# Performance work log

Measured on AMD Instinct MI355X. Metric: run time of the kernel, lower is better.

Reference implementation:

```python
import jax, jax.numpy as jnp
import numpy as np
from jax import lax

B, C, IMG, PATCH = 128, 3, 224, 16
EMB, HEADS = 384, 6
NPATCH = (IMG // PATCH) ** 2          # 196
NTOK = NPATCH + 1                     # 197 (cls token)
HID = int(EMB * 4.0)                  # 1536 (also expert hidden)
NE, K = 4, 2                          # num_experts (hardcoded 4), top-k
NCLS = 1000


def _ln(x, g, b, eps=1e-5):
    m = jnp.mean(x, axis=-1, keepdims=True)
    v = jnp.mean((x - m) ** 2, axis=-1, keepdims=True)
    return (x - m) * lax.rsqrt(v + eps) * g + b


def setup_inputs() -> dict:
    key = jax.random.key(0)
    ks = jax.random.split(key, 16)
    s = 0.02
    return {
        "x": jax.random.normal(ks[0], (B, C, IMG, IMG), jnp.float32),
        "conv_w": jax.random.normal(ks[1], (EMB, C, PATCH, PATCH), jnp.float32) * s,
        "conv_b": jnp.zeros((EMB,), jnp.float32),
        "cls_token": jax.random.normal(ks[2], (1, 1, EMB), jnp.float32) * s,
        "pos_embed": jax.random.normal(ks[3], (1, NTOK, EMB), jnp.float32) * s,
        "ln1_g": jnp.ones((EMB,), jnp.float32),
        "ln1_b": jnp.zeros((EMB,), jnp.float32),
        "in_proj_w": jax.random.normal(ks[4], (3 * EMB, EMB), jnp.float32) * s,
        "in_proj_b": jnp.zeros((3 * EMB,), jnp.float32),
        "out_proj_w": jax.random.normal(ks[5], (EMB, EMB), jnp.float32) * s,
        "out_proj_b": jnp.zeros((EMB,), jnp.float32),
        "router_w": jax.random.normal(ks[6], (NE, EMB), jnp.float32) * s,
        "router_b": jnp.zeros((NE,), jnp.float32),
        "ew1": jax.random.normal(ks[7], (NE, EMB, HID), jnp.float32) * s,
        "eb1": jnp.zeros((NE, HID), jnp.float32),
        "ew2": jax.random.normal(ks[8], (NE, HID, EMB), jnp.float32) * s,
        "eb2": jnp.zeros((NE, EMB), jnp.float32),
        "ln2_g": jnp.ones((EMB,), jnp.float32),
        "ln2_b": jnp.zeros((EMB,), jnp.float32),
        "head_w": jax.random.normal(ks[9], (NCLS, EMB), jnp.float32) * s,
        "head_b": jnp.zeros((NCLS,), jnp.float32),
    }


def reference(x, conv_w, conv_b, cls_token, pos_embed,
              ln1_g, ln1_b, in_proj_w, in_proj_b, out_proj_w, out_proj_b,
              router_w, router_b, ew1, eb1, ew2, eb2,
              ln2_g, ln2_b, head_w, head_b):
    # ---- patch embedding: Conv2d(stride=kernel=patch) -> [B, N, E]
    h = lax.conv_general_dilated(x, conv_w, window_strides=(PATCH, PATCH),
                                 padding="VALID",
                                 dimension_numbers=("NCHW", "OIHW", "NCHW"))
    h = h + conv_b[None, :, None, None]
    h = h.reshape(B, EMB, NPATCH).transpose(0, 2, 1)          # [B, 196, E]
    h = jnp.concatenate([jnp.broadcast_to(cls_token, (B, 1, EMB)), h], axis=1)
    h = h + pos_embed                                         # [B, 197, E]

    # ---- SelfAttentionBlock (NOTE: no residual; same LN applied twice, as in source)
    hn = _ln(h, ln1_g, ln1_b)
    qkv = hn @ in_proj_w.T + in_proj_b                        # [B, N, 3E]
    q, k, v = jnp.split(qkv, 3, axis=-1)
    hd = EMB // HEADS
    q = q.reshape(B, NTOK, HEADS, hd)
    k = k.reshape(B, NTOK, HEADS, hd)
    v = v.reshape(B, NTOK, HEADS, hd)
    att = jnp.einsum("bqhd,bkhd->bhqk", q, k) / np.sqrt(hd).astype(np.float32)
    att = jax.nn.softmax(att, axis=-1)
    o = jnp.einsum("bhqk,bkhd->bqhd", att, v).reshape(B, NTOK, EMB)
    o = o @ out_proj_w.T + out_proj_b
    h = _ln(o, ln1_g, ln1_b)                                  # second LN, same params

    # ---- MoE: dense all-expert FFN + top-k gather + mean
    scores = jax.nn.softmax(h @ router_w.T + router_b, axis=-1)   # [B, N, NE]
    topk_vals, topk_idx = lax.top_k(scores, K)                    # [B, N, K]
    flat = h.reshape(B * NTOK, EMB)
    eh = jax.nn.gelu(jnp.einsum("te,neh->tnh", flat, ew1) + eb1, approximate=False)
    eo = jnp.einsum("tnh,nhe->tne", eh, ew2) + eb2                # [BN, NE, E]
    idx = topk_idx.reshape(B * NTOK, K, 1)
    sel = jnp.take_along_axis(eo, idx, axis=1)                    # [BN, K, E]
    h = sel.mean(axis=1).reshape(B, NTOK, EMB)

    # ---- final norm + classification head on cls token
    h = _ln(h, ln2_g, ln2_b)
    return h[:, 0] @ head_w.T + head_b                            # [B, NCLS]
```

## Files before the change

kernel.cpp:

```cpp
#include <hip/hip_runtime.h>
#include <cstdint>
#include <cstddef>

typedef _Float16 f16;
typedef _Float16 f16x2 __attribute__((ext_vector_type(2)));
typedef _Float16 f16x8 __attribute__((ext_vector_type(8)));
typedef float    f32x4 __attribute__((ext_vector_type(4)));

constexpr int NTOKC  = 197;
constexpr int TTOK   = 128 * 197;
constexpr int EMB    = 384;
constexpr int HID    = 1536;

constexpr size_t OFF_CONVW   = 0;
constexpr size_t OFF_EW1T    = 1179648;
constexpr size_t OFF_EW2T    = 5898240;
constexpr size_t OFF_HEADW16 = 10616832;
constexpr size_t OFF_XCLS16  = 11403264;
constexpr size_t OFF_HCLS16  = 11799552;
constexpr size_t OFF_MASKW   = 11897856;
constexpr size_t OFF_EH      = 11899904;
constexpr size_t OFF_EPART   = 13472768;
constexpr size_t OFF_HFIN    = 16618496;
constexpr size_t OFF_XH      = 16716800;
constexpr size_t OFF_R       = 36082688;
constexpr size_t OFF_CVEC    = 36094976;
constexpr size_t OFF_U16     = 36099072;
constexpr size_t OFF_SG      = 38212608;
constexpr size_t OFF_SCLS    = 38817792;
constexpr size_t OFF_F       = 38818816;
constexpr size_t OFF_B2      = 40588288;
constexpr size_t OFF_FPART   = 40589824;
constexpr size_t WS_NEEDED   = 41769472;

__device__ __forceinline__ void gload16(const void* g, void* l) {
  __builtin_amdgcn_global_load_lds(
      (__attribute__((address_space(1))) void*)(void*)g,
      (__attribute__((address_space(3))) void*)l, 16, 0, 0);
}

#define PACK8(hv, p0, p1) { hv[0]=(f16)p0.x; hv[1]=(f16)p0.y; hv[2]=(f16)p0.z; hv[3]=(f16)p0.w; \
                            hv[4]=(f16)p1.x; hv[5]=(f16)p1.y; hv[6]=(f16)p1.z; hv[7]=(f16)p1.w; }

__global__ __launch_bounds__(256) void prep_all_k(
    const float* __restrict__ conv_w, const float* __restrict__ head_w,
    const float* __restrict__ ew1, const float* __restrict__ ew2,
    const float* __restrict__ inp_w, const float* __restrict__ inp_b,
    const float* __restrict__ outp_w, const float* __restrict__ outp_b,
    f16* __restrict__ convw, f16* __restrict__ headw16,
    f16* __restrict__ ew1t, f16* __restrict__ ew2t,
    f16* __restrict__ F, float* __restrict__ bias2) {
  __shared__ __attribute__((aligned(16))) char sbuf[4352];
  const int bx = (int)blockIdx.x, tid = threadIdx.x;
  if (bx < 2688) {
    int i = bx * 256 + tid;
    if (i < 294912) convw[i] = (f16)conv_w[i];
    int j = i - 294912;
    if (j >= 0 && j < 393216) {
      int row = j / 384;
      headw16[j] = (row < 1000) ? (f16)head_w[j] : (f16)0.f;
    }
  } else if (bx < 4992) {
    float (*tile)[33] = (float(*)[33])sbuf;
    int local = bx - 2688;
    int e = local / 576, r2 = local - e * 576;
    int byy = r2 / 48, bxx = r2 - byy * 48;
    const float* pin = ew1 + (size_t)e * 384 * 1536;
    f16* pout = ew1t + (size_t)e * 384 * 1536;
    int c0 = bxx * 32, r0 = byy * 32;
    int tx = tid & 31, ty = tid >> 5;
#pragma unroll
    for (int i = 0; i < 4; i++)
      tile[ty + 8 * i][tx] = pin[(size_t)(r0 + ty + 8 * i) * 1536 + c0 + tx];
    __syncthreads();
#pragma unroll
    for (int i = 0; i < 4; i++)
      pout[(size_t)(c0 + ty + 8 * i) * 384 + r0 + tx] = (f16)tile[tx][ty + 8 * i];
  } else if (bx < 7296) {
    float (*tile)[33] = (float(*)[33])sbuf;
    int local = bx - 4992;
    int e = local / 576, r2 = local - e * 576;
    int byy = r2 / 12, bxx = r2 - byy * 12;
    const float* pin = ew2 + (size_t)e * 1536 * 384;
    f16* pout = ew2t + (size_t)e * 1536 * 384;
    int c0 = bxx * 32, r0 = byy * 32;
    int tx = tid & 31, ty = tid >> 5;
#pragma unroll
    for (int i = 0; i < 4; i++)
      tile[ty + 8 * i][tx] = pin[(size_t)(r0 + ty + 8 * i) * 384 + c0 + tx];
    __syncthreads();
#pragma unroll
    for (int i = 0; i < 4; i++)
      pout[(size_t)(c0 + ty + 8 * i) * 1536 + r0 + tx] = (f16)tile[tx][ty + 8 * i];
  } else if (bx < 7440) {
    float (*wo)[64] = (float(*)[64])sbuf;
    int local = bx - 7296;
    int h = local / 24, nt = local - h * 24;
    int n0 = nt * 16;
    for (int i = tid; i < 1024; i += 256) {
      int ni = i >> 6, d = i & 63;
      wo[ni][d] = outp_w[(size_t)(n0 + ni) * 384 + h * 64 + d];
    }
    __syncthreads();
    for (int e = tid; e < 6144; e += 256) {
      int ni = e / 384, k2 = e - ni * 384;
      const float* wv = inp_w + (size_t)(768 + h * 64) * 384 + k2;
      float a = 0.f;
#pragma unroll 8
      for (int d = 0; d < 64; d++) a += wo[ni][d] * wv[(size_t)d * 384];
      F[(size_t)(n0 + ni) * 2304 + h * 384 + k2] = (f16)a;
    }
  } else {
    int nt = bx - 7440;
    if (tid < 16) {
      int n = nt * 16 + tid;
      const float* wrow = outp_w + (size_t)n * 384;
      float a = outp_b[n];
      for (int c = 0; c < 384; c++) a += wrow[c] * inp_b[768 + c];
      bias2[n] = a;
    }
  }
}

__global__ __launch_bounds__(384) void clsrprep_k(
    const float* __restrict__ cls, const float* __restrict__ posw,
    const float* __restrict__ g, const float* __restrict__ bb,
    const float* __restrict__ inp_w, const float* __restrict__ inp_b,
    f16* __restrict__ xcls16, float* __restrict__ Rg,
    float* __restrict__ Cg, float* __restrict__ Scls) {
  __shared__ float xs[EMB];
  __shared__ float red[16];
  __shared__ float qh[64];
  __shared__ float sred[6];
  const int h = (int)blockIdx.x, t = threadIdx.x;
  const int lane = t & 63, wave = t >> 6;
  float v = cls[t] + posw[t];
  float s = v, sq = v * v;
#pragma unroll
  for (int off = 32; off; off >>= 1) {
    s += __shfl_xor(s, off);
    sq += __shfl_xor(sq, off);
  }
  if (lane == 0) { red[wave] = s; red[8 + wave] = sq; }
  __syncthreads();
  float S = 0.f, SQ = 0.f;
#pragma unroll
  for (int i = 0; i < 6; i++) { S += red[i]; SQ += red[8 + i]; }
  float m = S * (1.f / 384.f);
  float rs = rsqrtf(SQ * (1.f / 384.f) - m * m + 1e-5f);
  float y = (v - m) * rs * g[t] + bb[t];
  xs[t] = y;
  xcls16[t] = (f16)y;
  __syncthreads();
  if (t < 64) {
    const float* wq = inp_w + (size_t)(h * 64 + t) * 384;
    float a = inp_b[h * 64 + t];
#pragma unroll 8
    for (int c = 0; c < 384; c++) a += wq[c] * xs[c];
    qh[t] = a;
  }
  __syncthreads();
  const float* wp = inp_w + (size_t)(384 + h * 64) * 384 + t;
  float a = 0.f;
#pragma unroll 8
  for (int d = 0; d < 64; d++) a += wp[(size_t)d * 384] * qh[d];
  Rg[h * 384 + t] = a;
  float part = a * xs[t];
#pragma unroll
  for (int off = 32; off; off >>= 1) part += __shfl_xor(part, off);
  if (lane == 0) sred[wave] = part;
  __syncthreads();
  if (t == 0) {
    float c = 0.f;
    for (int d = 0; d < 64; d++) c += qh[d] * inp_b[384 + h * 64 + d];
    Cg[h] = c;
    float st = c;
#pragma unroll
    for (int i = 0; i < 6; i++) st += sred[i];
    Scls[h] = st;
  }
}

__global__ __launch_bounds__(1024) void embed_ln_k(
    const float* __restrict__ img, const f16* __restrict__ B,
    const float* __restrict__ bias, const float* __restrict__ posw,
    const float* __restrict__ g, const float* __restrict__ bb,
    const float* __restrict__ Rg, const float* __restrict__ Cg,
    const f16* __restrict__ xcls16, const float* __restrict__ Scls,
    f16* __restrict__ xh, float* __restrict__ Sg) {
  __shared__ __attribute__((aligned(16))) char smem[57344];
  f16* As0 = (f16*)smem;
  f16* As1 = (f16*)(smem + 4096);
  f16* Bs0 = (f16*)(smem + 8192);
  f16* Bs1 = (f16*)(smem + 32768);
  const int K = 768;
  const int NT = 24;
  const int tid = threadIdx.x;
  const int lane = tid & 63;
  const int wave = tid >> 6;
  const int rowgrp = wave & 3;
  const int colgrp = wave >> 2;
  const int m0 = (int)blockIdx.x * 64;
  const int fr = lane & 15;
  const int fq = lane >> 4;

  if (blockIdx.x < 128) {
    if (tid < 384) xh[(size_t)blockIdx.x * NTOKC * EMB + tid] = xcls16[tid];
    if (tid < 6) Sg[((size_t)blockIdx.x * 6 + tid) * 197] = Scls[tid];
  }

  f32x4 acc[6];
#pragma unroll
  for (int j = 0; j < 6; j++) acc[j] = f32x4{0.f, 0.f, 0.f, 0.f};

  const int sr = lane >> 2, sc = (lane & 3) * 8;
  const int swzS = (((lane & 3) ^ (sr & 3)) * 8);
  const int swzR = ((fq ^ (fr & 3)) * 8);

  const float* abase = nullptr;
  int adoff = 0;
  if (wave < 4) {
    int row = m0 + wave * 16 + sr;
    int bimg = row / 196;
    int pp = row - bimg * 196;
    int py = pp / 14, px = pp - py * 14;
    int kx0 = sc & 15;
    abase = img + ((size_t)(bimg * 3) * 224 + py * 16) * 224 + px * 16 + kx0;
    adoff = (wave * 16 + sr) * 32 + swzS;
  }
  const f16* gb0 = nullptr;
  int lboff = 0;
  if (wave >= 4) {
    int brow = (wave - 4) * 32;
    gb0 = B + (size_t)(brow + sr) * K + swzS;
    lboff = brow * 32;
  }

  float4 a0x, a0y, a1x, a1y;
  if (wave < 4) {
    {
      int col = sc;
      const float* src = abase + (col >> 8) * 50176 + ((col >> 4) & 15) * 224;
      float4 p0 = *(const float4*)src;
      float4 p1 = *(const float4*)(src + 4);
      f16x8 hv; PACK8(hv, p0, p1);
      *(f16x8*)(As0 + adoff) = hv;
    }
    {
      int col = 32 + sc;
      const float* src = abase + (col >> 8) * 50176 + ((col >> 4) & 15) * 224;
      a0x = *(const float4*)src; a0y = *(const float4*)(src + 4);
    }
    {
      int col = 64 + sc;
      const float* src = abase + (col >> 8) * 50176 + ((col >> 4) & 15) * 224;
      a1x = *(const float4*)src; a1y = *(const float4*)(src + 4);
    }
  } else {
    gload16(gb0, Bs0 + lboff);
    gload16(gb0 + (size_t)16 * K, Bs0 + lboff + 16 * 32);
    gb0 += 32;
  }
  __syncthreads();

  f16* AsC = As0; f16* AsN = As1;
  f16* BsC = Bs0; f16* BsN = Bs1;

  for (int t = 0; t < NT; ++t) {
    if (wave < 4) {
      if (t + 1 < NT) {
        f16x8 hv;
        if ((t & 1) == 0) { PACK8(hv, a0x, a0y); }
        else              { PACK8(hv, a1x, a1y); }
        *(f16x8*)(AsN + adoff) = hv;
      }
      if (t + 3 < NT) {
        int col = (t + 3) * 32 + sc;
        const float* src = abase + (col >> 8) * 50176 + ((col >> 4) & 15) * 224;
        if ((t & 1) == 0) { a0x = *(const float4*)src; a0y = *(const float4*)(src + 4); }
        else              { a1x = *(const float4*)src; a1y = *(const float4*)(src + 4); }
      }
    } else {
      if (t + 1 < NT) {
        gload16(gb0, BsN + lboff);
        gload16(gb0 + (size_t)16 * K, BsN + lboff + 16 * 32);
        gb0 += 32;
      }
    }
    f16x8 af = *(const f16x8*)&AsC[(rowgrp * 16 + fr) * 32 + swzR];
#pragma unroll
    for (int j = 0; j < 6; j++) {
      f16x8 bf = *(const f16x8*)&BsC[(colgrp * 96 + j * 16 + fr) * 32 + swzR];
      acc[j] = __builtin_amdgcn_mfma_f32_16x16x32_f16(af, bf, acc[j], 0, 0, 0);
    }
    __syncthreads();
    f16* tA = AsC; AsC = AsN; AsN = tA;
    f16* tB = BsC; BsC = BsN; BsN = tB;
  }

  float* prm   = (float*)smem;
  float* psum  = (float*)(smem + 4608);
  float* pqsum = (float*)(smem + 5632);
  float* Rs2   = (float*)(smem + 6656);
  float* psc   = (float*)(smem + 15872);
  for (int i = tid; i < 1152; i += 1024)
    prm[i] = (i < 384) ? bias[i] : ((i < 768) ? g[i - 384] : bb[i - 768]);
  for (int i = tid; i < 2304; i += 1024) Rs2[i] = Rg[i];
  __syncthreads();

  float v[4][6];
#pragma unroll
  for (int rg = 0; rg < 4; rg++) {
    int lrow = rowgrp * 16 + fq * 4 + rg;
    int row = m0 + lrow;
    int bimg = row / 196;
    int pp = row - bimg * 196;
    const float* prow = posw + (size_t)(pp + 1) * EMB;
    float s = 0.f, sq = 0.f;
#pragma unroll
    for (int j = 0; j < 6; j++) {
      int col = colgrp * 96 + j * 16 + fr;
      float t = acc[j][rg] + prm[col] + prow[col];
      v[rg][j] = t;
      s += t; sq += t * t;
    }
#pragma unroll
    for (int off = 1; off < 16; off <<= 1) {
      s += __shfl_xor(s, off);
      sq += __shfl_xor(sq, off);
    }
    if (fr == 0) { psum[lrow * 4 + colgrp] = s; pqsum[lrow * 4 + colgrp] = sq; }
  }
  __syncthreads();

#pragma unroll
  for (int rg = 0; rg < 4; rg++) {
    int lrow = rowgrp * 16 + fq * 4 + rg;
    float S = psum[lrow * 4] + psum[lrow * 4 + 1] + psum[lrow * 4 + 2] + psum[lrow * 4 + 3];
    float SQ = pqsum[lrow * 4] + pqsum[lrow * 4 + 1] + pqsum[lrow * 4 + 2] + pqsum[lrow * 4 + 3];
    float m = S * (1.f / 384.f);
    float rs = rsqrtf(SQ * (1.f / 384.f) - m * m + 1e-5f);
    int row = m0 + lrow;
    int bimg = row / 196;
    int pp = row - bimg * 196;
    f16* orow = xh + ((size_t)bimg * NTOKC + pp + 1) * EMB;
#pragma unroll
    for (int j = 0; j < 6; j++) {
      int col = colgrp * 96 + j * 16 + fr;
      float y = (v[rg][j] - m) * rs * prm[384 + col] + prm[768 + col];
      v[rg][j] = y;
      orow[col] = (f16)y;
    }
  }

#pragma unroll
  for (int h = 0; h < 6; h++) {
    float rv[6];
#pragma unroll
    for (int j = 0; j < 6; j++)
      rv[j] = Rs2[h * 384 + colgrp * 96 + j * 16 + fr];
#pragma unroll
    for (int rg = 0; rg < 4; rg++) {
      float p = v[rg][0] * rv[0] + v[rg][1] * rv[1] + v[rg][2] * rv[2]
              + v[rg][3] * rv[3] + v[rg][4] * rv[4] + v[rg][5] * rv[5];
#pragma unroll
      for (int off = 1; off < 16; off <<= 1) p += __shfl_xor(p, off);
      if (fr == 0) psc[(rowgrp * 16 + fq * 4 + rg) * 24 + colgrp * 6 + h] = p;
    }
  }
  __syncthreads();
  if (tid < 384) {
    int lrow = tid / 6, h = tid - lrow * 6;
    float s = psc[lrow * 24 + h] + psc[lrow * 24 + 6 + h]
            + psc[lrow * 24 + 12 + h] + psc[lrow * 24 + 18 + h] + Cg[h];
    int row = m0 + lrow;
    int bimg = row / 196, pp = row - bimg * 196;
    Sg[((size_t)bimg * 6 + h) * 197 + pp + 1] = s;
  }
}

__global__ __launch_bounds__(512) void u_gemv_k(
    const float* __restrict__ Sg, const f16* __restrict__ xh,
    f16* __restrict__ U16) {
  __shared__ float pf[6 * 208];
  __shared__ float part[8][64][12];
  const int cq = (int)blockIdx.x;
  const int b  = (int)blockIdx.y;
  const int tid = threadIdx.x;
  const int wave = tid >> 6, lane = tid & 63;

  if (wave < 6) {
    const float* sp = Sg + ((size_t)b * 6 + wave) * 197;
    float z[4], pk[4];
#pragma unroll
    for (int k = 0; k < 4; k++) {
      int t = lane + 64 * k;
      z[k] = (t < 197) ? sp[t] * 0.125f : -1e30f;
      pk[k] = 0.f;
    }
    float mx = fmaxf(fmaxf(z[0], z[1]), fmaxf(z[2], z[3]));
#pragma unroll
    for (int off = 32; off; off >>= 1) mx = fmaxf(mx, __shfl_xor(mx, off));
    float sum = 0.f;
#pragma unroll
    for (int k = 0; k < 4; k++) {
      int t = lane + 64 * k;
      if (t < 197) {
        pk[k] = __expf(z[k] - mx);
        sum += pk[k];
      }
    }
#pragma unroll
    for (int off = 32; off; off >>= 1) sum += __shfl_xor(sum, off);
    float si = 1.f / sum;
#pragma unroll
    for (int k = 0; k < 4; k++) {
      int t = lane + 64 * k;
      if (t < 208) pf[wave * 208 + t] = pk[k] * si;
    }
  }
  __syncthreads();

  const int cp = tid & 63;
  const int tq = tid >> 6;
  const int col0 = cq * 128 + cp * 2;
  const int t0 = 25 * tq;
  const int t1 = (t0 + 25 < 197) ? t0 + 25 : 197;
  float acc[12];
#pragma unroll
  for (int r = 0; r < 12; r++) acc[r] = 0.f;
  const f16* xp = xh + ((size_t)b * NTOKC + t0) * EMB + col0;
#pragma unroll 4
  for (int t = t0; t < t1; t++) {
    f16x2 xv = *(const f16x2*)xp;
    float x0 = (float)xv[0];
    float x1 = (float)xv[1];
    xp += EMB;
#pragma unroll
    for (int h = 0; h < 6; h++) {
      float p = pf[h * 208 + t];
      acc[h * 2]     += p * x0;
      acc[h * 2 + 1] += p * x1;
    }
  }
#pragma unroll
  for (int r = 0; r < 12; r++) part[tq][cp][r] = acc[r];
  __syncthreads();
  for (int idx = tid; idx < 768; idx += 512) {
    int cp2 = idx / 12, slot = idx - cp2 * 12;
    int h = slot >> 1, c01 = slot & 1;
    float u = 0.f;
#pragma unroll
    for (int q = 0; q < 8; q++) u += part[q][cp2][slot];
    U16[(size_t)b * 2304 + h * 384 + cq * 128 + cp2 * 2 + c01] = (f16)u;
  }
}

__global__ __launch_bounds__(256) void fproj_k(
    const f16* __restrict__ U16, const f16* __restrict__ F,
    float* __restrict__ fpart) {
  __shared__ f16 As[128 * 32];
  __shared__ f16 Bs[64 * 32];
  const int tid = threadIdx.x;
  const int lane = tid & 63;
  const int wave = tid >> 6;
  const int n0 = (int)blockIdx.x * 64;
  const int kc = (int)blockIdx.y;
  const int wm = (wave >> 1) * 64;
  const int wn = (wave & 1) * 32;
  const int fr = lane & 15;
  const int fq = lane >> 4;

  f32x4 acc[4][2];
#pragma unroll
  for (int i = 0; i < 4; i++)
#pragma unroll
    for (int j = 0; j < 2; j++) acc[i][j] = f32x4{0.f, 0.f, 0.f, 0.f};

  const int sr = lane >> 2;
  const int sc = (lane & 3) * 8;
  const f16* ag = U16 + (size_t)(wave * 32 + sr) * 2304 + kc * 384 + sc;
  const f16* bg = F + (size_t)(n0 + wave * 16 + sr) * 2304 + kc * 384 + sc;
  const size_t rstep = (size_t)16 * 2304;
  f16* la = As + wave * 32 * 32;
  f16* lb = Bs + wave * 16 * 32;

  for (int k0 = 0; k0 < 384; k0 += 32) {
    gload16(ag, la);  gload16(ag + rstep, la + 16 * 32);
    gload16(bg, lb);
    ag += 32; bg += 32;
    __syncthreads();
    f16x8 af[4], bf[2];
#pragma unroll
    for (int i = 0; i < 4; i++)
      af[i] = *(const f16x8*)&As[(wm + i * 16 + fr) * 32 + fq * 8];
#pragma unroll
    for (int j = 0; j < 2; j++)
      bf[j] = *(const f16x8*)&Bs[(wn + j * 16 + fr) * 32 + fq * 8];
#pragma unroll
    for (int i = 0; i < 4; i++)
#pragma unroll
      for (int j = 0; j < 2; j++)
        acc[i][j] = __builtin_amdgcn_mfma_f32_16x16x32_f16(af[i], bf[j], acc[i][j], 0, 0, 0);
    __syncthreads();
  }

#pragma unroll
  for (int i = 0; i < 4; i++)
#pragma unroll
    for (int j = 0; j < 2; j++)
#pragma unroll
      for (int rg = 0; rg < 4; rg++) {
        int gm = wm + i * 16 + fq * 4 + rg;
        int gn = n0 + wn + j * 16 + fr;
        fpart[((size_t)kc * 128 + gm) * EMB + gn] = acc[i][j][rg];
      }
}

__global__ __launch_bounds__(384) void ln_router_k(
    const float* __restrict__ fpart, const float* __restrict__ bias2,
    const float* __restrict__ g, const float* __restrict__ bb,
    const float* __restrict__ rw, const float* __restrict__ rb,
    f16* __restrict__ hcls16, float* __restrict__ maskw) {
  __shared__ float red[16];
  __shared__ float part[6][4];
  __shared__ float logits[4];
  int b = blockIdx.x, t = threadIdx.x;
  int lane = t & 63, wave = t >> 6;
  float v = bias2[t];
#pragma unroll
  for (int kc = 0; kc < 6; kc++)
    v += fpart[((size_t)kc * 128 + b) * EMB + t];
  float s = v, sq = v * v;
#pragma unroll
  for (int off = 32; off; off >>= 1) {
    s += __shfl_xor(s, off);
    sq += __shfl_xor(sq, off);
  }
  if (lane == 0) { red[wave] = s; red[8 + wave] = sq; }
  __syncthreads();
  float S = 0.f, SQ = 0.f;
#pragma unroll
  for (int i = 0; i < 6; i++) { S += red[i]; SQ += red[8 + i]; }
  float m = S * (1.f / 384.f);
  float rs = rsqrtf(SQ * (1.f / 384.f) - m * m + 1e-5f);
  float y = (v - m) * rs * g[t] + bb[t];
  hcls16[(size_t)b * EMB + t] = (f16)y;
  float p0 = y * rw[t];
  float p1 = y * rw[EMB + t];
  float p2 = y * rw[2 * EMB + t];
  float p3 = y * rw[3 * EMB + t];
#pragma unroll
  for (int off = 32; off; off >>= 1) {
    p0 += __shfl_xor(p0, off);
    p1 += __shfl_xor(p1, off);
    p2 += __shfl_xor(p2, off);
    p3 += __shfl_xor(p3, off);
  }
  if (lane == 0) { part[wave][0] = p0; part[wave][1] = p1; part[wave][2] = p2; part[wave][3] = p3; }
  __syncthreads();
  if (t < 4) {
    float a = rb[t];
#pragma unroll
    for (int i = 0; i < 6; i++) a += part[i][t];
    logits[t] = a;
  }
  __syncthreads();
  if (t == 0) {
    float l0 = logits[0], l1 = logits[1], l2 = logits[2], l3 = logits[3];
    int i1 = 0; float b1 = l0;
    if (l1 > b1) { b1 = l1; i1 = 1; }
    if (l2 > b1) { b1 = l2; i1 = 2; }
    if (l3 > b1) { b1 = l3; i1 = 3; }
    int i2 = -1; float b2 = 0.f;
    float lv[4] = {l0, l1, l2, l3};
#pragma unroll
    for (int i = 0; i < 4; i++) {
      if (i == i1) continue;
      if (i2 < 0 || lv[i] > b2) { i2 = i; b2 = lv[i]; }
    }
#pragma unroll
    for (int e = 0; e < 4; e++)
      maskw[(size_t)b * 4 + e] = (e == i1 || e == i2) ? 0.5f : 0.f;
  }
}

__global__ __launch_bounds__(256) void moe1_k(
    const f16* __restrict__ A, const f16* __restrict__ Bm,
    const float* __restrict__ bias, f16* __restrict__ outh) {
  __shared__ f16 As[128 * 32];
  __shared__ f16 Bs[64 * 32];
  const int K = EMB;
  const int tid = threadIdx.x;
  const int lane = tid & 63;
  const int wave = tid >> 6;
  const int e = (int)blockIdx.y;
  const int n0 = (int)blockIdx.x * 64;
  const int wm = (wave >> 1) * 64;
  const int wn = (wave & 1) * 32;
  const int fr = lane & 15;
  const int fq = lane >> 4;
  Bm += (size_t)e * HID * EMB;
  bias += (size_t)e * HID;

  f32x4 acc[4][2];
#pragma unroll
  for (int i = 0; i < 4; i++)
#pragma unroll
    for (int j = 0; j < 2; j++) acc[i][j] = f32x4{0.f, 0.f, 0.f, 0.f};

  const int sr = lane >> 2;
  const int sc = (lane & 3) * 8;
  const f16* ag = A + (size_t)(wave * 32 + sr) * K + sc;
  const f16* bg = Bm + (size_t)(n0 + wave * 16 + sr) * K + sc;
  const size_t rstep = (size_t)16 * K;
  f16* la = As + wave * 32 * 32;
  f16* lb = Bs + wave * 16 * 32;

  for (int k0 = 0; k0 < K; k0 += 32) {
    gload16(ag, la);  gload16(ag + rstep, la + 16 * 32);
    gload16(bg, lb);
    ag += 32; bg += 32;
    __syncthreads();
    f16x8 af[4], bf[2];
#pragma unroll
    for (int i = 0; i < 4; i++)
      af[i] = *(const f16x8*)&As[(wm + i * 16 + fr) * 32 + fq * 8];
#pragma unroll
    for (int j = 0; j < 2; j++)
      bf[j] = *(const f16x8*)&Bs[(wn + j * 16 + fr) * 32 + fq * 8];
#pragma unroll
    for (int i = 0; i < 4; i++)
#pragma unroll
      for (int j = 0; j < 2; j++)
        acc[i][j] = __builtin_amdgcn_mfma_f32_16x16x32_f16(af[i], bf[j], acc[i][j], 0, 0, 0);
    __syncthreads();
  }

#pragma unroll
  for (int i = 0; i < 4; i++)
#pragma unroll
    for (int j = 0; j < 2; j++)
#pragma unroll
      for (int rg = 0; rg < 4; rg++) {
        int gm = wm + i * 16 + fq * 4 + rg;
        int gn = n0 + wn + j * 16 + fr;
        float v = acc[i][j][rg] + bias[gn];
        float gl = 0.5f * v * (1.0f + erff(v * 0.70710678118654752f));
        outh[(size_t)e * 128 * HID + (size_t)gm * HID + gn] = (f16)gl;
      }
}

__global__ __launch_bounds__(256) void moe2_k(
    const f16* __restrict__ EH, const f16* __restrict__ W2,
    float* __restrict__ part) {
  __shared__ f16 As[128 * 32];
  __shared__ f16 Bs[64 * 32];
  const int tid = threadIdx.x;
  const int lane = tid & 63;
  const int wave = tid >> 6;
  const int n0 = (int)blockIdx.x * 64;
  const int e = (int)blockIdx.y;
  const int kc = (int)blockIdx.z;
  const int wm = (wave >> 1) * 64;
  const int wn = (wave & 1) * 32;
  const int fr = lane & 15;
  const int fq = lane >> 4;
  const f16* A = EH + (size_t)e * 128 * HID + kc * 384;
  const f16* B = W2 + (size_t)e * EMB * HID + kc * 384;

  f32x4 acc[4][2];
#pragma unroll
  for (int i = 0; i < 4; i++)
#pragma unroll
    for (int j = 0; j < 2; j++) acc[i][j] = f32x4{0.f, 0.f, 0.f, 0.f};

  const int sr = lane >> 2;
  const int sc = (lane & 3) * 8;
  const f16* ag = A + (size_t)(wave * 32 + sr) * HID + sc;
  const f16* bg = B + (size_t)(n0 + wave * 16 + sr) * HID + sc;
  const size_t rstep = (size_t)16 * HID;
  f16* la = As + wave * 32 * 32;
  f16* lb = Bs + wave * 16 * 32;

  for (int k0 = 0; k0 < 384; k0 += 32) {
    gload16(ag, la);  gload16(ag + rstep, la + 16 * 32);
    gload16(bg, lb);
    ag += 32; bg += 32;
    __syncthreads();
    f16x8 af[4], bf[2];
#pragma unroll
    for (int i = 0; i < 4; i++)
      af[i] = *(const f16x8*)&As[(wm + i * 16 + fr) * 32 + fq * 8];
#pragma unroll
    for (int j = 0; j < 2; j++)
      bf[j] = *(const f16x8*)&Bs[(wn + j * 16 + fr) * 32 + fq * 8];
#pragma unroll
    for (int i = 0; i < 4; i++)
#pragma unroll
      for (int j = 0; j < 2; j++)
        acc[i][j] = __builtin_amdgcn_mfma_f32_16x16x32_f16(af[i], bf[j], acc[i][j], 0, 0, 0);
    __syncthreads();
  }

#pragma unroll
  for (int i = 0; i < 4; i++)
#pragma unroll
    for (int j = 0; j < 2; j++)
#pragma unroll
      for (int rg = 0; rg < 4; rg++) {
        int gm = wm + i * 16 + fq * 4 + rg;
        int gn = n0 + wn + j * 16 + fr;
        part[(((size_t)kc * 4 + e) * 128 + gm) * EMB + gn] = acc[i][j][rg];
      }
}

__global__ __launch_bounds__(384) void combine_ln2_k(
    const float* __restrict__ part, const float* __restrict__ eb2,
    const float* __restrict__ maskw,
    const float* __restrict__ g, const float* __restrict__ bb,
    f16* __restrict__ hfin) {
  __shared__ float red[16];
  int b = blockIdx.x, t = threadIdx.x;
  int lane = t & 63, wave = t >> 6;
  float v = 0.f;
#pragma unroll
  for (int e = 0; e < 4; e++) {
    float s = eb2[e * EMB + t];
#pragma unroll
    for (int kc = 0; kc < 4; kc++)
      s += part[(((size_t)kc * 4 + e) * 128 + b) * EMB + t];
    v += maskw[b * 4 + e] * s;
  }
  float s = v, sq = v * v;
#pragma unroll
  for (int off = 32; off; off >>= 1) {
    s += __shfl_xor(s, off);
    sq += __shfl_xor(sq, off);
  }
  if (lane == 0) { red[wave] = s; red[8 + wave] = sq; }
  __syncthreads();
  float S = 0.f, SQ = 0.f;
#pragma unroll
  for (int i = 0; i < 6; i++) { S += red[i]; SQ += red[8 + i]; }
  float m = S * (1.f / 384.f);
  float rs = rsqrtf(SQ * (1.f / 384.f) - m * m + 1e-5f);
  hfin[(size_t)b * EMB + t] = (f16)((v - m) * rs * g[t] + bb[t]);
}

__global__ __launch_bounds__(256) void head_gemm_k(
    const f16* __restrict__ A, const f16* __restrict__ B,
    const float* __restrict__ hb, float* __restrict__ outp) {
  __shared__ f16 As[128 * 32];
  __shared__ f16 Bs[64 * 32];
  const int K = 384;
  const int tid = threadIdx.x;
  const int lane = tid & 63;
  const int wave = tid >> 6;
  const int n0 = (int)blockIdx.x * 64;
  const int wm = (wave >> 1) * 64;
  const int wn = (wave & 1) * 32;
  const int fr = lane & 15;
  const int fq = lane >> 4;

  f32x4 acc[4][2];
#pragma unroll
  for (int i = 0; i < 4; i++)
#pragma unroll
    for (int j = 0; j < 2; j++) acc[i][j] = f32x4{0.f, 0.f, 0.f, 0.f};

  const int sr = lane >> 2;
  const int sc = (lane & 3) * 8;
  const f16* ag = A + (size_t)(wave * 32 + sr) * K + sc;
  const f16* bg = B + (size_t)(n0 + wave * 16 + sr) * K + sc;
  const size_t rstep = (size_t)16 * K;
  f16* la = As + wave * 32 * 32;
  f16* lb = Bs + wave * 16 * 32;

  for (int k0 = 0; k0 < K; k0 += 32) {
    gload16(ag, la);  gload16(ag + rstep, la + 16 * 32);
    gload16(bg, lb);
    ag += 32; bg += 32;
    __syncthreads();
    f16x8 af[4], bf[2];
#pragma unroll
    for (int i = 0; i < 4; i++)
      af[i] = *(const f16x8*)&As[(wm + i * 16 + fr) * 32 + fq * 8];
#pragma unroll
    for (int j = 0; j < 2; j++)
      bf[j] = *(const f16x8*)&Bs[(wn + j * 16 + fr) * 32 + fq * 8];
#pragma unroll
    for (int i = 0; i < 4; i++)
#pragma unroll
      for (int j = 0; j < 2; j++)
        acc[i][j] = __builtin_amdgcn_mfma_f32_16x16x32_f16(af[i], bf[j], acc[i][j], 0, 0, 0);
    __syncthreads();
  }

#pragma unroll
  for (int i = 0; i < 4; i++)
#pragma unroll
    for (int j = 0; j < 2; j++)
#pragma unroll
      for (int rg = 0; rg < 4; rg++) {
        int gm = wm + i * 16 + fq * 4 + rg;
        int gn = n0 + wn + j * 16 + fr;
        if (gn < 1000)
          outp[(size_t)gm * 1000 + gn] = acc[i][j][rg] + hb[gn];
      }
}

extern "C" void kernel_launch(void* const* d_in, const int* in_sizes, int n_in,
                              void* d_out, int out_size, void* d_ws, size_t ws_size,
                              hipStream_t stream) {
  const float* x      = (const float*)d_in[0];
  const float* conv_w = (const float*)d_in[1];
  const float* conv_b = (const float*)d_in[2];
  const float* cls_t  = (const float*)d_in[3];
  const float* pos    = (const float*)d_in[4];
  const float* ln1_g  = (const float*)d_in[5];
  const float* ln1_b  = (const float*)d_in[6];
  const float* inp_w  = (const float*)d_in[7];
  const float* inp_b  = (const float*)d_in[8];
  const float* outp_w = (const float*)d_in[9];
  const float* outp_b = (const float*)d_in[10];
  const float* rt_w   = (const float*)d_in[11];
  const float* rt_b   = (const float*)d_in[12];
  const float* ew1    = (const float*)d_in[13];
  const float* eb1    = (const float*)d_in[14];
  const float* ew2    = (const float*)d_in[15];
  const float* eb2    = (const float*)d_in[16];
  const float* ln2_g  = (const float*)d_in[17];
  const float* ln2_b  = (const float*)d_in[18];
  const float* head_w = (const float*)d_in[19];
  const float* head_b = (const float*)d_in[20];
  float* out = (float*)d_out;
  char* w = (char*)d_ws;
  if (ws_size < WS_NEEDED) return;

  f16* convw    = (f16*)(w + OFF_CONVW);
  f16* ew1t     = (f16*)(w + OFF_EW1T);
  f16* ew2t     = (f16*)(w + OFF_EW2T);
  f16* headw16  = (f16*)(w + OFF_HEADW16);
  f16* xcls16   = (f16*)(w + OFF_XCLS16);
  f16* hcls16   = (f16*)(w + OFF_HCLS16);
  float* maskw  = (float*)(w + OFF_MASKW);
  f16* ehbuf    = (f16*)(w + OFF_EH);
  float* epart  = (float*)(w + OFF_EPART);
  f16* hfin     = (f16*)(w + OFF_HFIN);
  f16* xh       = (f16*)(w + OFF_XH);
  float* Rg     = (float*)(w + OFF_R);
  float* Cg     = (float*)(w + OFF_CVEC);
  f16* u16      = (f16*)(w + OFF_U16);
  float* sg     = (float*)(w + OFF_SG);
  float* scls   = (float*)(w + OFF_SCLS);
  f16* Fw       = (f16*)(w + OFF_F);
  float* bias2  = (float*)(w + OFF_B2);
  float* fpart  = (float*)(w + OFF_FPART);

  prep_all_k<<<dim3(7464), 256, 0, stream>>>(
      conv_w, head_w, ew1, ew2, inp_w, inp_b, outp_w, outp_b,
      convw, headw16, ew1t, ew2t, Fw, bias2);

  clsrprep_k<<<dim3(6), 384, 0, stream>>>(
      cls_t, pos, ln1_g, ln1_b, inp_w, inp_b, xcls16, Rg, Cg, scls);

  embed_ln_k<<<dim3(392), 1024, 0, stream>>>(
      x, convw, conv_b, pos, ln1_g, ln1_b, Rg, Cg, xcls16, scls, xh, sg);

  u_gemv_k<<<dim3(3, 128), 512, 0, stream>>>(sg, xh, u16);

  fproj_k<<<dim3(6, 6), 256, 0, stream>>>(u16, Fw, fpart);
  ln_router_k<<<dim3(128), 384, 0, stream>>>(
      fpart, bias2, ln1_g, ln1_b, rt_w, rt_b, hcls16, maskw);

  moe1_k<<<dim3(24, 4), 256, 0, stream>>>(hcls16, ew1t, eb1, ehbuf);
  moe2_k<<<dim3(6, 4, 4), 256, 0, stream>>>(ehbuf, ew2t, epart);
  combine_ln2_k<<<dim3(128), 384, 0, stream>>>(epart, eb2, maskw, ln2_g, ln2_b, hfin);

  head_gemm_k<<<dim3(16), 256, 0, stream>>>(hfin, headw16, head_b, out);
  (void)in_sizes; (void)n_in; (void)out_size;
}
```

Before: 338.9 us.

## Double-buffer LDS tiles in MFMA GEMMs and register-cache weight columns in fusion prep

Each of the four small MFMA GEMM kernels (fproj, moe1, moe2, head) now uses two LDS buffers per operand. The next k-tile load is issued before computing on the current tile, which removes one barrier per iteration and lets the global-to-LDS copies overlap the MFMAs. The prep kernel that builds the fused V/out-projection matrix now loads each input-weight column into registers once and reuses it across 16 output rows, instead of rereading it from global memory for every row. The cost is double the LDS footprint per block and heavy register use from the 64-float column array, which could lower occupancy.

```diff
diff --git a/kernel.cpp b/kernel.cpp
--- a/kernel.cpp
+++ b/kernel.cpp
@@ -102,13 +102,18 @@
       wo[ni][d] = outp_w[(size_t)(n0 + ni) * 384 + h * 64 + d];
     }
     __syncthreads();
-    for (int e = tid; e < 6144; e += 256) {
-      int ni = e / 384, k2 = e - ni * 384;
+    for (int k2 = tid; k2 < 384; k2 += 256) {
       const float* wv = inp_w + (size_t)(768 + h * 64) * 384 + k2;
-      float a = 0.f;
-#pragma unroll 8
-      for (int d = 0; d < 64; d++) a += wo[ni][d] * wv[(size_t)d * 384];
-      F[(size_t)(n0 + ni) * 2304 + h * 384 + k2] = (f16)a;
+      float wcol[64];
+#pragma unroll
+      for (int d = 0; d < 64; d++) wcol[d] = wv[(size_t)d * 384];
+#pragma unroll
+      for (int ni = 0; ni < 16; ni++) {
+        float a = 0.f;
+#pragma unroll
+        for (int d = 0; d < 64; d++) a += wo[ni][d] * wcol[d];
+        F[(size_t)(n0 + ni) * 2304 + h * 384 + k2] = (f16)a;
+      }
     }
   } else {
     int nt = bx - 7440;
@@ -459,8 +464,8 @@
 __global__ __launch_bounds__(256) void fproj_k(
     const f16* __restrict__ U16, const f16* __restrict__ F,
     float* __restrict__ fpart) {
-  __shared__ f16 As[128 * 32];
-  __shared__ f16 Bs[64 * 32];
+  __shared__ f16 As[2][128 * 32];
+  __shared__ f16 Bs[2][64 * 32];
   const int tid = threadIdx.x;
   const int lane = tid & 63;
   const int wave = tid >> 6;
@@ -482,27 +487,35 @@
   const f16* ag = U16 + (size_t)(wave * 32 + sr) * 2304 + kc * 384 + sc;
   const f16* bg = F + (size_t)(n0 + wave * 16 + sr) * 2304 + kc * 384 + sc;
   const size_t rstep = (size_t)16 * 2304;
-  f16* la = As + wave * 32 * 32;
-  f16* lb = Bs + wave * 16 * 32;
-
+  const int laoff = wave * 32 * 32 + sr * 32 + sc;
+  const int lboff = wave * 16 * 32 + sr * 32 + sc;
+
+  gload16(ag, &As[0][laoff]); gload16(ag + rstep, &As[0][laoff + 16 * 32]);
+  gload16(bg, &Bs[0][lboff]);
+  ag += 32; bg += 32;
+  __syncthreads();
+
+  int cur = 0;
   for (int k0 = 0; k0 < 384; k0 += 32) {
-    gload16(ag, la);  gload16(ag + rstep, la + 16 * 32);
-    gload16(bg, lb);
-    ag += 32; bg += 32;
-    __syncthreads();
+    if (k0 + 32 < 384) {
+      gload16(ag, &As[cur ^ 1][laoff]); gload16(ag + rstep, &As[cur ^ 1][laoff + 16 * 32]);
+      gload16(bg, &Bs[cur ^ 1][lboff]);
+      ag += 32; bg += 32;
+    }
     f16x8 af[4], bf[2];
 #pragma unroll
     for (int i = 0; i < 4; i++)
-      af[i] = *(const f16x8*)&As[(wm + i * 16 + fr) * 32 + fq * 8];
+      af[i] = *(const f16x8*)&As[cur][(wm + i * 16 + fr) * 32 + fq * 8];
 #pragma unroll
     for (int j = 0; j < 2; j++)
-      bf[j] = *(const f16x8*)&Bs[(wn + j * 16 + fr) * 32 + fq * 8];
+      bf[j] = *(const f16x8*)&Bs[cur][(wn + j * 16 + fr) * 32 + fq * 8];
 #pragma unroll
     for (int i = 0; i < 4; i++)
 #pragma unroll
       for (int j = 0; j < 2; j++)
         acc[i][j] = __builtin_amdgcn_mfma_f32_16x16x32_f16(af[i], bf[j], acc[i][j], 0, 0, 0);
     __syncthreads();
+    cur ^= 1;
   }
 
 #pragma unroll
@@ -588,8 +601,8 @@
 __global__ __launch_bounds__(256) void moe1_k(
     const f16* __restrict__ A, const f16* __restrict__ Bm,
     const float* __restrict__ bias, f16* __restrict__ outh) {
-  __shared__ f16 As[128 * 32];
-  __shared__ f16 Bs[64 * 32];
+  __shared__ f16 As[2][128 * 32];
+  __shared__ f16 Bs[2][64 * 32];
   const int K = EMB;
   const int tid = threadIdx.x;
   const int lane = tid & 63;
@@ -614,27 +627,35 @@
   const f16* ag = A + (size_t)(wave * 32 + sr) * K + sc;
   const f16* bg = Bm + (size_t)(n0 + wave * 16 + sr) * K + sc;
   const size_t rstep = (size_t)16 * K;
-  f16* la = As + wave * 32 * 32;
-  f16* lb = Bs + wave * 16 * 32;
-
+  const int laoff = wave * 32 * 32 + sr * 32 + sc;
+  const int lboff = wave * 16 * 32 + sr * 32 + sc;
+
+  gload16(ag, &As[0][laoff]); gload16(ag + rstep, &As[0][laoff + 16 * 32]);
+  gload16(bg, &Bs[0][lboff]);
+  ag += 32; bg += 32;
+  __syncthreads();
+
+  int cur = 0;
   for (int k0 = 0; k0 < K; k0 += 32) {
-    gload16(ag, la);  gload16(ag + rstep, la + 16 * 32);
-    gload16(bg, lb);
-    ag += 32; bg += 32;
-    __syncthreads();
+    if (k0 + 32 < K) {
+      gload16(ag, &As[cur ^ 1][laoff]); gload16(ag + rstep, &As[cur ^ 1][laoff + 16 * 32]);
+      gload16(bg, &Bs[cur ^ 1][lboff]);
+      ag += 32; bg += 32;
+    }
     f16x8 af[4], bf[2];
 #pragma unroll
     for (int i = 0; i < 4; i++)
-      af[i] = *(const f16x8*)&As[(wm + i * 16 + fr) * 32 + fq * 8];
+      af[i] = *(const f16x8*)&As[cur][(wm + i * 16 + fr) * 32 + fq * 8];
 #pragma unroll
     for (int j = 0; j < 2; j++)
-      bf[j] = *(const f16x8*)&Bs[(wn + j * 16 + fr) * 32 + fq * 8];
+      bf[j] = *(const f16x8*)&Bs[cur][(wn + j * 16 + fr) * 32 + fq * 8];
 #pragma unroll
     for (int i = 0; i < 4; i++)
 #pragma unroll
       for (int j = 0; j < 2; j++)
         acc[i][j] = __builtin_amdgcn_mfma_f32_16x16x32_f16(af[i], bf[j], acc[i][j], 0, 0, 0);
     __syncthreads();
+    cur ^= 1;
   }
 
 #pragma unroll
@@ -654,8 +675,8 @@
 __global__ __launch_bounds__(256) void moe2_k(
     const f16* __restrict__ EH, const f16* __restrict__ W2,
     float* __restrict__ part) {
-  __shared__ f16 As[128 * 32];
-  __shared__ f16 Bs[64 * 32];
+  __shared__ f16 As[2][128 * 32];
+  __shared__ f16 Bs[2][64 * 32];
   const int tid = threadIdx.x;
   const int lane = tid & 63;
   const int wave = tid >> 6;
@@ -680,27 +701,35 @@
   const f16* ag = A + (size_t)(wave * 32 + sr) * HID + sc;
   const f16* bg = B + (size_t)(n0 + wave * 16 + sr) * HID + sc;
   const size_t rstep = (size_t)16 * HID;
-  f16* la = As + wave * 32 * 32;
-  f16* lb = Bs + wave * 16 * 32;
-
+  const int laoff = wave * 32 * 32 + sr * 32 + sc;
+  const int lboff = wave * 16 * 32 + sr * 32 + sc;
+
+  gload16(ag, &As[0][laoff]); gload16(ag + rstep, &As[0][laoff + 16 * 32]);
+  gload16(bg, &Bs[0][lboff]);
+  ag += 32; bg += 32;
+  __syncthreads();
+
+  int cur = 0;
   for (int k0 = 0; k0 < 384; k0 += 32) {
-    gload16(ag, la);  gload16(ag + rstep, la + 16 * 32);
-    gload16(bg, lb);
-    ag += 32; bg += 32;
-    __syncthreads();
+    if (k0 + 32 < 384) {
+      gload16(ag, &As[cur ^ 1][laoff]); gload16(ag + rstep, &As[cur ^ 1][laoff + 16 * 32]);
+      gload16(bg, &Bs[cur ^ 1][lboff]);
+      ag += 32; bg += 32;
+    }
     f16x8 af[4], bf[2];
 #pragma unroll
     for (int i = 0; i < 4; i++)
-      af[i] = *(const f16x8*)&As[(wm + i * 16 + fr) * 32 + fq * 8];
+      af[i] = *(const f16x8*)&As[cur][(wm + i * 16 + fr) * 32 + fq * 8];
 #pragma unroll
     for (int j = 0; j < 2; j++)
-      bf[j] = *(const f16x8*)&Bs[(wn + j * 16 + fr) * 32 + fq * 8];
+      bf[j] = *(const f16x8*)&Bs[cur][(wn + j * 16 + fr) * 32 + fq * 8];
 #pragma unroll
     for (int i = 0; i < 4; i++)
 #pragma unroll
       for (int j = 0; j < 2; j++)
         acc[i][j] = __builtin_amdgcn_mfma_f32_16x16x32_f16(af[i], bf[j], acc[i][j], 0, 0, 0);
     __syncthreads();
+    cur ^= 1;
   }
 
 #pragma unroll
@@ -751,8 +780,8 @@
 __global__ __launch_bounds__(256) void head_gemm_k(
     const f16* __restrict__ A, const f16* __restrict__ B,
     const float* __restrict__ hb, float* __restrict__ outp) {
-  __shared__ f16 As[128 * 32];
-  __shared__ f16 Bs[64 * 32];
+  __shared__ f16 As[2][128 * 32];
+  __shared__ f16 Bs[2][64 * 32];
   const int K = 384;
   const int tid = threadIdx.x;
   const int lane = tid & 63;
@@ -774,27 +803,35 @@
   const f16* ag = A + (size_t)(wave * 32 + sr) * K + sc;
   const f16* bg = B + (size_t)(n0 + wave * 16 + sr) * K + sc;
   const size_t rstep = (size_t)16 * K;
-  f16* la = As + wave * 32 * 32;
-  f16* lb = Bs + wave * 16 * 32;
-
+  const int laoff = wave * 32 * 32 + sr * 32 + sc;
+  const int lboff = wave * 16 * 32 + sr * 32 + sc;
+
+  gload16(ag, &As[0][laoff]); gload16(ag + rstep, &As[0][laoff + 16 * 32]);
+  gload16(bg, &Bs[0][lboff]);
+  ag += 32; bg += 32;
+  __syncthreads();
+
+  int cur = 0;
   for (int k0 = 0; k0 < K; k0 += 32) {
-    gload16(ag, la);  gload16(ag + rstep, la + 16 * 32);
-    gload16(bg, lb);
-    ag += 32; bg += 32;
-    __syncthreads();
+    if (k0 + 32 < K) {
+      gload16(ag, &As[cur ^ 1][laoff]); gload16(ag + rstep, &As[cur ^ 1][laoff + 16 * 32]);
+      gload16(bg, &Bs[cur ^ 1][lboff]);
+      ag += 32; bg += 32;
+    }
     f16x8 af[4], bf[2];
 #pragma unroll
     for (int i = 0; i < 4; i++)
-      af[i] = *(const f16x8*)&As[(wm + i * 16 + fr) * 32 + fq * 8];
+      af[i] = *(const f16x8*)&As[cur][(wm + i * 16 + fr) * 32 + fq * 8];
 #pragma unroll
     for (int j = 0; j < 2; j++)
-      bf[j] = *(const f16x8*)&Bs[(wn + j * 16 + fr) * 32 + fq * 8];
+      bf[j] = *(const f16x8*)&Bs[cur][(wn + j * 16 + fr) * 32 + fq * 8];
 #pragma unroll
     for (int i = 0; i < 4; i++)
 #pragma unroll
       for (int j = 0; j < 2; j++)
         acc[i][j] = __builtin_amdgcn_mfma_f32_16x16x32_f16(af[i], bf[j], acc[i][j], 0, 0, 0);
     __syncthreads();
+    cur ^= 1;
   }
 
 #pragma unroll
```

Measured after the change: 340.7 us. About the same (+0.5%).
